# Performance work log

Hardware: AMD Instinct MI355X
Metric: run time of the kernel (lower is better)

Reference implementation:

```python
import jax, jax.numpy as jnp
import numpy as np

B, L, H, E = 4, 2048, 8, 64
WINDOW = 8
DILATION = 1


def setup_inputs() -> dict:
    key = jax.random.key(0)
    kq, kk, kv, ka = jax.random.split(key, 4)
    queries = jax.random.normal(kq, (B, L, H, E), dtype=jnp.float32)
    keys = jax.random.normal(kk, (B, L, H, E), dtype=jnp.float32)
    values = jax.random.normal(kv, (B, L, H, E), dtype=jnp.float32)
    alpha = jax.random.uniform(ka, (1,), dtype=jnp.float32)
    return {"queries": queries, "keys": keys, "values": values, "alpha": alpha}


def _full_attention(q, k, v, scale):
    # q,k,v: [B, L, H, E]
    scores = jnp.einsum('blhe,bshe->bhls', q, k) * scale  # [B,H,L,L]
    A = jax.nn.softmax(scores, axis=-1)
    return jnp.einsum('bhls,bshd->blhd', A, v)


def _local_attention(q, k, v, scale):
    # efficient gather-based local window attention, non-causal
    Lk = k.shape[1]
    offsets = jnp.arange(-WINDOW, WINDOW + 1) * DILATION
    idx = jnp.clip(jnp.arange(Lk)[:, None] + offsets[None, :], 0, Lk - 1)
    K_win = k[:, idx]
    V_win = v[:, idx]
    scores = jnp.einsum('blhe,blwhe->blhw', q, K_win) * scale
    A = jax.nn.softmax(scores, axis=-1)
    return jnp.einsum('blhw,blwhe->blhe', A, V_win)


def reference(queries, keys, values, alpha):
    scale = 1.0 / np.sqrt(queries.shape[-1]).astype(np.float32)
    out_full = _full_attention(queries, keys, values, scale)
    out_local = _local_attention(queries, keys, values, scale)
    w = jax.nn.sigmoid(alpha[0])
    # only_target_first=True: positions 1..L-1 take out_full, position 0 is gated
    out = out_full.at[:, 0].set(w * out_full[:, 0] + (1.0 - w) * out_local[:, 0])
    return out
```

## Files before the change

### kernel.cpp

```cpp
#include <hip/hip_runtime.h>

typedef unsigned short u16;
typedef unsigned int   u32;
typedef __attribute__((ext_vector_type(8))) short short8;
typedef __attribute__((ext_vector_type(16))) float f32x16;

#define MFMA32(a, b, c) __builtin_amdgcn_mfma_f32_32x32x16_bf16(a, b, c, 0, 0, 0)

constexpr int Lv = 2048, Hv = 8, Ev = 64, HE = Hv * Ev;
constexpr float QSCALE = 0.18033688011112042f;
constexpr size_t WSV_OFF = 32u * 64u * 2048u;
#define WS_NEED ((size_t)16777216)

__device__ __forceinline__ float bf2f(u16 u) {
    u32 x = ((u32)u) << 16;
    return __builtin_bit_cast(float, x);
}
__device__ __forceinline__ u16 f2bf(float f) {
    u32 x = __builtin_bit_cast(u32, f);
    u32 r = ((x >> 16) & 1u) + 0x7fffu;
    return (u16)((x + r) >> 16);
}
__device__ __forceinline__ u32 pkbf(float a, float b) {
#if __has_builtin(__builtin_amdgcn_cvt_pk_bf16_f32)
    typedef __attribute__((ext_vector_type(2))) __bf16 bf16x2;
    bf16x2 v = __builtin_amdgcn_cvt_pk_bf16_f32(a, b);
    return __builtin_bit_cast(u32, v);
#else
    return (u32)f2bf(a) | ((u32)f2bf(b) << 16);
#endif
}
__device__ __forceinline__ float fexp2(float x) {
#if __has_builtin(__builtin_amdgcn_exp2f)
    return __builtin_amdgcn_exp2f(x);
#else
    return exp2f(x);
#endif
}

__device__ __forceinline__ void gll16(const void* g, void* l) {
    __builtin_amdgcn_global_load_lds(
        (const __attribute__((address_space(1))) void*)g,
        (__attribute__((address_space(3))) void*)l, 16, 0, 0);
}

__device__ __forceinline__ int detect_isbf16(const u32* q32, int lane) {
    u32 w0 = q32[2 * lane];
    u32 w1 = q32[2 * lane + 1];
    u16 uu[4] = { (u16)(w0 & 0xffff), (u16)(w0 >> 16),
                  (u16)(w1 & 0xffff), (u16)(w1 >> 16) };
    int p = 0, z = 0;
#pragma unroll
    for (int j = 0; j < 4; ++j) {
        u16 mgn = (u16)(uu[j] & 0x7fff);
        int ex  = mgn >> 7;
        bool zero = (mgn == 0);
        bool pl   = zero || (ex >= 115 && ex <= 132);
        p += pl ? 1 : 0;
        if ((j & 1) == 0) z += zero ? 1 : 0;
    }
    int acc = p | (z << 16);
#pragma unroll
    for (int o = 1; o < 64; o <<= 1) acc += __shfl_xor(acc, o);
    int ps = acc & 0xffff, zs = acc >> 16;
    if (zs >= 100) return 0;
    return (ps >= 240) ? 1 : 0;
}

__device__ __forceinline__ short8 cvt8s(const float* p, float s) {
    float4 a = *(const float4*)p, b4 = *(const float4*)(p + 4);
    u32 r[4] = { pkbf(a.x * s, a.y * s), pkbf(a.z * s, a.w * s),
                 pkbf(b4.x * s, b4.y * s), pkbf(b4.z * s, b4.w * s) };
    return *(short8*)r;
}

__device__ __forceinline__ f32x16 zv16() {
    f32x16 z;
#pragma unroll
    for (int r = 0; r < 16; ++r) z[r] = 0.f;
    return z;
}

__device__ __forceinline__ void plswap(u32& a, u32& b) {
#if __has_builtin(__builtin_amdgcn_permlane32_swap)
    auto r = __builtin_amdgcn_permlane32_swap(a, b, false, false);
    a = r[0]; b = r[1];
#else
    int lane = (int)(threadIdx.x & 63);
    u32 ax = (u32)__shfl_xor((int)a, 32);
    u32 bx = (u32)__shfl_xor((int)b, 32);
    bool hi = lane >= 32;
    u32 na = hi ? bx : a;
    u32 nb = hi ? b  : ax;
    a = na; b = nb;
#endif
}

template <int ISBF>
__device__ __forceinline__ void convert_impl(const void* kin, const void* vin,
                                             u16* __restrict__ ws, u16* VT) {
    const int blk = blockIdx.x;
    const int xcd = blk & 7;
    const int bh  = xcd * 4 + ((blk >> 3) & 3);
    const int tg  = blk >> 5;
    const int b   = bh >> 3, h = bh & 7;
    const size_t inb = (size_t)b * Lv * HE + h * Ev;
    u16* kimg = ws + ((size_t)bh * 64 + tg) * 2048;
    u16* vimg = ws + WSV_OFF + ((size_t)bh * 64 + tg) * 2048;
    const int t = threadIdx.x;

    if (ISBF) {
        int key = t >> 3, p8 = t & 7;
        size_t src = inb + (size_t)(tg * 32 + key) * HE + p8 * 8;
        uint4 v = *(const uint4*)((const u16*)vin + src);
        *(uint4*)&VT[key * 72 + p8 * 8] = v;
    } else {
#pragma unroll
        for (int r = 0; r < 2; ++r) {
            int f = t + 256 * r;
            int key = f >> 4, part = f & 15;
            size_t src = inb + (size_t)(tg * 32 + key) * HE + part * 4;
            float4 v = *(const float4*)((const float*)vin + src);
            uint2 pv; pv.x = pkbf(v.x, v.y); pv.y = pkbf(v.z, v.w);
            *(uint2*)&VT[key * 72 + part * 4] = pv;
        }
    }

    {
        int a = 8 * t;
        int key = a >> 6, sf = (a & 63) >> 3;
        int e0 = ((sf ^ (key & 7)) << 3);
        size_t s = inb + (size_t)(tg * 32 + key) * HE + e0;
        if (ISBF) {
            uint4 v = *(const uint4*)((const u16*)kin + s);
            *(uint4*)&kimg[a] = v;
        } else {
            float4 p0 = *(const float4*)((const float*)kin + s);
            float4 p1 = *(const float4*)((const float*)kin + s + 4);
            uint4 v; v.x = pkbf(p0.x, p0.y); v.y = pkbf(p0.z, p0.w);
                     v.z = pkbf(p1.x, p1.y); v.w = pkbf(p1.z, p1.w);
            *(uint4*)&kimg[a] = v;
        }
    }

    __syncthreads();

#pragma unroll
    for (int r = 0; r < 2; ++r) {
        int idx = t + 256 * r;
        int a = 4 * idx;
        int e = a >> 5, sf = (a & 31) >> 3, j0 = a & 7;
        int m = (e + (e >> 3)) & 3;
        int k0 = ((sf ^ m) << 3) + j0;
        uint2 val;
        val.x = (u32)VT[k0 * 72 + e]       | ((u32)VT[(k0 + 1) * 72 + e] << 16);
        val.y = (u32)VT[(k0 + 2) * 72 + e] | ((u32)VT[(k0 + 3) * 72 + e] << 16);
        *(uint2*)&vimg[a] = val;
    }
}

__global__ __launch_bounds__(256) void convert_kernel(
    const void* __restrict__ qv, const void* __restrict__ kv,
    const void* __restrict__ vv, u16* __restrict__ ws)
{
    __shared__ u16 VT[32 * 72];
    const int isbf = detect_isbf16((const u32*)qv, threadIdx.x & 63);
    if (isbf) convert_impl<1>(kv, vv, ws, VT);
    else      convert_impl<0>(kv, vv, ws, VT);
}

template <int ISBF, int WS>
__device__ __forceinline__ void attn_impl(
    const void* __restrict__ qv, const void* __restrict__ kv,
    const void* __restrict__ vv, const void* __restrict__ alphav,
    void* __restrict__ outv, const u16* __restrict__ ws, u16* SMEM)
{
    const int tid  = threadIdx.x;
    const int w    = tid >> 6;
    const int lane = tid & 63;
    const int l31  = lane & 31;
    const int hi   = lane >> 5;
    const int qg   = w & 3;
    const int g    = w >> 2;

    const int fid = blockIdx.x;
    const int bh  = (fid & 7) * 4 + ((fid >> 3) & 3);
    const int rb  = fid >> 5;
    const int b   = bh >> 3, h = bh & 7;
    const int row0 = rb * 128;

    const size_t bhoff = (size_t)b * Lv * HE + h * Ev;
    const u16*   q16 = (const u16*)qv + bhoff;
    const u16*   k16 = (const u16*)kv + bhoff;
    const u16*   v16 = (const u16*)vv + bhoff;
    const float* q32 = (const float*)qv + bhoff;
    const float* k32 = (const float*)kv + bhoff;
    const float* v32 = (const float*)vv + bhoff;

    u16* ldsK = SMEM + w * 4096;
    u16* ldsV = ldsK + 2048;

    short8 qf[4];
    {
        size_t ro = (size_t)(row0 + qg * 32 + l31) * HE + hi * 8;
        if (ISBF) {
#pragma unroll
            for (int c = 0; c < 4; ++c) {
                short8 t = *(const short8*)(q16 + ro + 16 * c);
#pragma unroll
                for (int j = 0; j < 8; ++j)
                    qf[c][j] = (short)f2bf(bf2f((u16)t[j]) * QSCALE);
            }
        } else {
#pragma unroll
            for (int c = 0; c < 4; ++c) qf[c] = cvt8s(q32 + ro + 16 * c, QSCALE);
        }
    }

    f32x16 O[2];
    O[0] = zv16(); O[1] = zv16();
    f32x16 StA = zv16(), StB = zv16();
    float psum = 0.f;

    const u16* kimg0 = ws + ((size_t)bh * 64 + g * 32) * 2048;
    const u16* vimg0 = ws + WSV_OFF + ((size_t)bh * 64 + g * 32) * 2048;
    const size_t keybase = (size_t)g * 1024;

    const int k0l = lane >> 3;
    const int kj  = lane & 7;
    const int e0K = ((kj ^ k0l) << 3);
    const int eoV = kj * 8;

    float4 fpa, fpb, fpc, fpd;
    uint4  upa, upb;

#define GLLK(KT) do {                                                          \
        const u16* ib_ = kimg0 + (size_t)(KT) * 2048 + lane * 8;               \
        _Pragma("unroll")                                                      \
        for (int s_ = 0; s_ < 4; ++s_)                                         \
            gll16(ib_ + s_ * 512, ldsK + s_ * 512);                            \
    } while (0)
#define GLLV(KT) do {                                                          \
        const u16* ib_ = vimg0 + (size_t)(KT) * 2048 + lane * 8;               \
        _Pragma("unroll")                                                      \
        for (int s_ = 0; s_ < 4; ++s_)                                         \
            gll16(ib_ + s_ * 512, ldsV + s_ * 512);                            \
    } while (0)
#define WAITV4() do { asm volatile("s_waitcnt vmcnt(4)" ::: "memory");         \
        __builtin_amdgcn_sched_barrier(0); } while (0)
#define WAITV0() do { asm volatile("s_waitcnt vmcnt(0)" ::: "memory");         \
        __builtin_amdgcn_sched_barrier(0); } while (0)
#define WAITL0() do { asm volatile("s_waitcnt lgkmcnt(0)" ::: "memory");       \
        __builtin_amdgcn_sched_barrier(0); } while (0)

#define LK0(KT, CH) do {                                                       \
        size_t tb_ = (keybase + (size_t)(KT) * 32) * HE;                       \
        int key_ = (CH) * 16 + k0l;                                            \
        if (ISBF) {                                                            \
            const u16* p_ = k16 + tb_ + (size_t)key_ * HE + e0K;               \
            upa = *(const uint4*)p_;                                           \
            upb = *(const uint4*)(p_ + 8 * HE);                                \
        } else {                                                               \
            const float* p_ = k32 + tb_ + (size_t)key_ * HE + e0K;             \
            fpa = *(const float4*)p_;            fpb = *(const float4*)(p_ + 4);\
            fpc = *(const float4*)(p_ + 8 * HE); fpd = *(const float4*)(p_ + 8 * HE + 4);\
        }                                                                      \
    } while (0)
#define SK0(CH) do {                                                           \
        if (ISBF) {                                                            \
            *(uint4*)&ldsK[((CH)*2    ) * 512 + lane * 8] = upa;               \
            *(uint4*)&ldsK[((CH)*2 + 1) * 512 + lane * 8] = upb;               \
        } else {                                                               \
            u32 t0_[4] = { pkbf(fpa.x, fpa.y), pkbf(fpa.z, fpa.w),             \
                           pkbf(fpb.x, fpb.y), pkbf(fpb.z, fpb.w) };           \
            u32 t1_[4] = { pkbf(fpc.x, fpc.y), pkbf(fpc.z, fpc.w),             \
                           pkbf(fpd.x, fpd.y), pkbf(fpd.z, fpd.w) };           \
            *(uint4*)&ldsK[((CH)*2    ) * 512 + lane * 8] = *(uint4*)t0_;      \
            *(uint4*)&ldsK[((CH)*2 + 1) * 512 + lane * 8] = *(uint4*)t1_;      \
        }                                                                      \
    } while (0)
#define LV0(KT, VH) do {                                                       \
        size_t tb_ = (keybase + (size_t)(KT) * 32 + (VH) * 16 + 2 * k0l) * HE; \
        if (ISBF) {                                                            \
            const u16* p_ = v16 + tb_ + eoV;                                   \
            upa = *(const uint4*)p_;                                           \
            upb = *(const uint4*)(p_ + HE);                                    \
        } else {                                                               \
            const float* p_ = v32 + tb_ + eoV;                                 \
            fpa = *(const float4*)p_;       fpb = *(const float4*)(p_ + 4);    \
            fpc = *(const float4*)(p_ + HE); fpd = *(const float4*)(p_ + HE + 4);\
        }                                                                      \
    } while (0)
#define SV0(VH) do {                                                           \
        int s_ = (k0l >> 2) + (VH) * 2;                                        \
        if (ISBF) {                                                            \
            const u16* a0_ = (const u16*)&upa;                                 \
            const u16* a1_ = (const u16*)&upb;                                 \
            _Pragma("unroll")                                                  \
            for (int j = 0; j < 8; ++j) {                                      \
                int e_ = eoV + j;                                              \
                int sl_ = s_ ^ ((e_ + (e_ >> 3)) & 3);                         \
                *(u32*)&ldsV[e_ * 32 + sl_ * 8 + ((2 * k0l) & 7)] =            \
                    (u32)a0_[j] | ((u32)a1_[j] << 16);                         \
            }                                                                  \
        } else {                                                               \
            float t0_[8] = {fpa.x, fpa.y, fpa.z, fpa.w, fpb.x, fpb.y, fpb.z, fpb.w};\
            float t1_[8] = {fpc.x, fpc.y, fpc.z, fpc.w, fpd.x, fpd.y, fpd.z, fpd.w};\
            _Pragma("unroll")                                                  \
            for (int j = 0; j < 8; ++j) {                                      \
                int e_ = eoV + j;                                              \
                int sl_ = s_ ^ ((e_ + (e_ >> 3)) & 3);                         \
                *(u32*)&ldsV[e_ * 32 + sl_ * 8 + ((2 * k0l) & 7)] =            \
                    pkbf(t0_[j], t1_[j]);                                      \
            }                                                                  \
        }                                                                      \
    } while (0)

#define QK_(ST) do {                                                           \
        (ST) = zv16();                                                         \
        __builtin_amdgcn_s_setprio(1);                                         \
        _Pragma("unroll")                                                      \
        for (int c = 0; c < 4; ++c) {                                          \
            int sl = (2 * c + hi) ^ (l31 & 7);                                 \
            short8 kf = *(const short8*)&ldsK[l31 * 64 + sl * 8];              \
            (ST) = MFMA32(kf, qf[c], (ST));                                    \
        }                                                                      \
        __builtin_amdgcn_s_setprio(0);                                         \
    } while (0)

    u32 c8[8];
#define SM_(SP) do {                                                           \
        _Pragma("unroll")                                                      \
        for (int r = 0; r < 16; ++r) (SP)[r] = fexp2((SP)[r]);                 \
        _Pragma("unroll")                                                      \
        for (int r = 0; r < 16; ++r) psum += (SP)[r];                          \
        _Pragma("unroll")                                                      \
        for (int q = 0; q < 8; ++q) c8[q] = pkbf((SP)[2 * q], (SP)[2 * q + 1]);\
    } while (0)

#define PV_(T) do {                                                            \
        u32 a0 = c8[4 * (T) + 0], a1 = c8[4 * (T) + 1];                        \
        u32 a2 = c8[4 * (T) + 2], a3 = c8[4 * (T) + 3];                        \
        plswap(a0, a2);                                                        \
        plswap(a1, a3);                                                        \
        u32 pw_[4] = { a0, a1, a2, a3 };                                       \
        short8 pa = *(short8*)pw_;                                             \
        __builtin_amdgcn_s_setprio(1);                                         \
        _Pragma("unroll")                                                      \
        for (int et = 0; et < 2; ++et) {                                       \
            int e  = et * 32 + l31;                                            \
            int sl = (2 * (T) + hi) ^ ((e + (e >> 3)) & 3);                    \
            short8 vf = *(const short8*)&ldsV[e * 32 + sl * 8];                \
            O[et] = MFMA32(pa, vf, O[et]);                                     \
        }                                                                      \
        __builtin_amdgcn_s_setprio(0);                                         \
    } while (0)

#define BODY(KT, SC, SP) do {                                                  \
        WAITV4();                   \
        QK_(SC);                    \
        SM_(SP);                    \
        WAITL0();                   \
        GLLK((KT) + 1);                                                        \
        WAITV4();                   \
        PV_(0);                                                                \
        PV_(1);                     \
        WAITL0();                   \
        GLLV(KT);                                                              \
    } while (0)

    if (WS) {
        GLLK(0);
        WAITV0();
        QK_(StA);
        WAITL0();
        GLLK(1);
        GLLV(0);
        for (int j = 0; j < 15; ++j) {
            const int kt = 2 * j + 1;
            BODY(kt,     StB, StA);
            BODY(kt + 1, StA, StB);
        }
        WAITV4();
        QK_(StB);
        SM_(StA);
        WAITL0();
        WAITV0();
        PV_(0);
        PV_(1);
        WAITL0();
        GLLV(31);
        WAITV0();
        SM_(StB);
        PV_(0);
        PV_(1);
    } else {
        LK0(0, 0); SK0(0); LK0(0, 1); SK0(1);
        LV0(0, 0); SV0(0); LV0(0, 1); SV0(1);
        for (int kt = 0; kt < 32; ++kt) {
            if (kt < 31) LK0(kt + 1, 0);
            QK_(StA);
            if (kt < 31) { SK0(0); LK0(kt + 1, 1); }
            SM_(StA);
            if (kt < 31) { SK0(1); LV0(kt + 1, 0); }
            PV_(0);
            if (kt < 31) { SV0(0); LV0(kt + 1, 1); }
            PV_(1);
            if (kt < 31) SV0(1);
        }
    }
#undef GLLK
#undef GLLV
#undef WAITV4
#undef WAITV0
#undef WAITL0
#undef LK0
#undef SK0
#undef LV0
#undef SV0
#undef QK_
#undef SM_
#undef PV_
#undef BODY

    __syncthreads();
    float pst = psum + __shfl_xor(psum, 32);
    float* cb = (float*)SMEM;
    const int cbase = qg * 2368 + lane * 36;

    if (g == 1) {
        union { f32x16 v; float4 q4[4]; } u;
        u.v = O[0];
#pragma unroll
        for (int i = 0; i < 4; ++i) *(float4*)&cb[cbase + 4 * i] = u.q4[i];
        u.v = O[1];
#pragma unroll
        for (int i = 0; i < 4; ++i) *(float4*)&cb[cbase + 16 + 4 * i] = u.q4[i];
        cb[qg * 2368 + 2304 + lane] = pst;
    }

    float locv[2] = {0.f, 0.f};
    float wgt = 0.f;
    const bool w0blk = (rb == 0) && (w == 0);
    if (w0blk) {
        const int e = lane;
        const size_t base = bhoff + e;
#define LDIN(p, i) (ISBF ? bf2f(((const u16*)(p))[i]) : ((const float*)(p))[i])
        float qe = LDIN(qv, base);
        float s[9];
#pragma unroll
        for (int j = 0; j < 9; ++j) {
            float prod = qe * LDIN(kv, base + (size_t)j * HE);
#pragma unroll
            for (int o = 1; o < 64; o <<= 1) prod += __shfl_xor(prod, o);
            s[j] = prod * 0.125f;
        }
        float mx = s[0];
#pragma unroll
        for (int j = 1; j < 9; ++j) mx = fmaxf(mx, s[j]);
        float we[9];
#pragma unroll
        for (int j = 0; j < 9; ++j) we[j] = expf(s[j] - mx);
        float denom = 9.f * we[0];
        float acc   = 9.f * we[0] * LDIN(vv, base);
#pragma unroll
        for (int j = 1; j < 9; ++j) {
            denom += we[j];
            acc   += we[j] * LDIN(vv, base + (size_t)j * HE);
        }
        float loc = acc / denom;

        float a;
        if (ISBF) {
            a = bf2f(((const u16*)alphav)[0]);
            if (!(a >= 0.0f && a <= 1.0f)) {
                float af = ((const float*)alphav)[0];
                if (af >= 0.0f && af <= 1.0f) a = af;
            }
        } else {
            a = ((const float*)alphav)[0];
            if (!(a >= 0.0f && a <= 1.0f)) {
                float ab = bf2f(((const u16*)alphav)[0]);
                if (ab >= 0.0f && ab <= 1.0f) a = ab;
            }
        }
        wgt = 1.f / (1.f + expf(-a));
#pragma unroll
        for (int et = 0; et < 2; ++et) locv[et] = __shfl(loc, et * 32 + l31);
#undef LDIN
    }

    __syncthreads();
    if (g != 0) return;

    float pstp = cb[qg * 2368 + 2304 + lane];
#pragma unroll
    for (int r = 0; r < 16; ++r) {
        O[0][r] += cb[cbase + r];
        O[1][r] += cb[cbase + 16 + r];
    }
    float invv = 1.0f / (pst + pstp);

#pragma unroll
    for (int rg = 0; rg < 4; ++rg) {
#pragma unroll
        for (int rr = 0; rr < 4; ++rr) {
            const int reg = rg * 4 + rr;
            const int rl  = rr + 8 * rg + 4 * hi;
            float inv = __shfl(invv, rl);
            int row = row0 + qg * 32 + rl;
            size_t oo = (size_t)(b * Lv + row) * HE + h * Ev + l31;
            bool blend = w0blk && (rl == 0);
#pragma unroll
            for (int et = 0; et < 2; ++et) {
                float res = O[et][reg] * inv;
                if (blend) res = wgt * res + (1.f - wgt) * locv[et];
                if (ISBF) ((u16*)outv)[oo + et * 32] = f2bf(res);
                else      ((float*)outv)[oo + et * 32] = res;
            }
        }
    }
}

__global__ __launch_bounds__(512, 4) void attn_kernel_ws(
    const void* __restrict__ qv, const void* __restrict__ kv,
    const void* __restrict__ vv, const void* __restrict__ alphav,
    void* __restrict__ outv, const u16* __restrict__ ws)
{
    __shared__ u16 SMEM[32768];
    const int isbf = detect_isbf16((const u32*)qv, threadIdx.x & 63);
    if (isbf) attn_impl<1, 1>(qv, kv, vv, alphav, outv, ws, SMEM);
    else      attn_impl<0, 1>(qv, kv, vv, alphav, outv, ws, SMEM);
}

__global__ __launch_bounds__(512, 4) void attn_kernel_nws(
    const void* __restrict__ qv, const void* __restrict__ kv,
    const void* __restrict__ vv, const void* __restrict__ alphav,
    void* __restrict__ outv)
{
    __shared__ u16 SMEM[32768];
    const int isbf = detect_isbf16((const u32*)qv, threadIdx.x & 63);
    if (isbf) attn_impl<1, 0>(qv, kv, vv, alphav, outv, nullptr, SMEM);
    else      attn_impl<0, 0>(qv, kv, vv, alphav, outv, nullptr, SMEM);
}

extern "C" void kernel_launch(void* const* d_in, const int* in_sizes, int n_in,
                              void* d_out, int out_size, void* d_ws, size_t ws_size,
                              hipStream_t stream) {
    if (d_ws != nullptr && ws_size >= WS_NEED) {
        hipLaunchKernelGGL(convert_kernel, dim3(2048), dim3(256), 0, stream,
                           d_in[0], d_in[1], d_in[2], (u16*)d_ws);
        hipLaunchKernelGGL(attn_kernel_ws, dim3(512), dim3(512), 0, stream,
                           d_in[0], d_in[1], d_in[2], d_in[3], d_out,
                           (const u16*)d_ws);
    } else {
        hipLaunchKernelGGL(attn_kernel_nws, dim3(512), dim3(512), 0, stream,
                           d_in[0], d_in[1], d_in[2], d_in[3], d_out);
    }
}
```

Before: 146.5 us.

## Fuse K/V conversion and attention into one cooperative kernel with grid sync

```diff
diff --git a/kernel.cpp b/kernel.cpp
--- a/kernel.cpp
+++ b/kernel.cpp
@@ -1,4 +1,5 @@
 #include <hip/hip_runtime.h>
+#include <hip/hip_cooperative_groups.h>
 
 typedef unsigned short u16;
 typedef unsigned int   u32;
@@ -96,67 +97,67 @@
 #endif
 }
 
-template <int ISBF>
-__device__ __forceinline__ void convert_impl(const void* kin, const void* vin,
-                                             u16* __restrict__ ws, u16* VT) {
-    const int blk = blockIdx.x;
-    const int xcd = blk & 7;
-    const int bh  = xcd * 4 + ((blk >> 3) & 3);
-    const int tg  = blk >> 5;
-    const int b   = bh >> 3, h = bh & 7;
-    const size_t inb = (size_t)b * Lv * HE + h * Ev;
-    u16* kimg = ws + ((size_t)bh * 64 + tg) * 2048;
-    u16* vimg = ws + WSV_OFF + ((size_t)bh * 64 + tg) * 2048;
-    const int t = threadIdx.x;
-
-    if (ISBF) {
-        int key = t >> 3, p8 = t & 7;
-        size_t src = inb + (size_t)(tg * 32 + key) * HE + p8 * 8;
-        uint4 v = *(const uint4*)((const u16*)vin + src);
-        *(uint4*)&VT[key * 72 + p8 * 8] = v;
-    } else {
-#pragma unroll
-        for (int r = 0; r < 2; ++r) {
-            int f = t + 256 * r;
-            int key = f >> 4, part = f & 15;
-            size_t src = inb + (size_t)(tg * 32 + key) * HE + part * 4;
-            float4 v = *(const float4*)((const float*)vin + src);
-            uint2 pv; pv.x = pkbf(v.x, v.y); pv.y = pkbf(v.z, v.w);
-            *(uint2*)&VT[key * 72 + part * 4] = pv;
-        }
-    }
-
-    {
-        int a = 8 * t;
-        int key = a >> 6, sf = (a & 63) >> 3;
-        int e0 = ((sf ^ (key & 7)) << 3);
+
+template <int ISBF, int NT>
+__device__ __forceinline__ void conv_tile(const void* kin, const void* vin,
+                                          size_t inb, int tg,
+                                          u16* __restrict__ kdst,
+                                          u16* __restrict__ vimg,
+                                          u16* __restrict__ VTt, int tl) {
+#pragma unroll
+    for (int r = 0; r < 2048 / (8 * NT); ++r) {
+        int a = 8 * (tl + NT * r);
+        int key = a >> 6, e0 = a & 63;
         size_t s = inb + (size_t)(tg * 32 + key) * HE + e0;
         if (ISBF) {
-            uint4 v = *(const uint4*)((const u16*)kin + s);
-            *(uint4*)&kimg[a] = v;
+            *(uint4*)&kdst[a] = *(const uint4*)((const u16*)kin + s);
         } else {
             float4 p0 = *(const float4*)((const float*)kin + s);
             float4 p1 = *(const float4*)((const float*)kin + s + 4);
             uint4 v; v.x = pkbf(p0.x, p0.y); v.y = pkbf(p0.z, p0.w);
                      v.z = pkbf(p1.x, p1.y); v.w = pkbf(p1.z, p1.w);
-            *(uint4*)&kimg[a] = v;
-        }
-    }
-
+            *(uint4*)&kdst[a] = v;
+        }
+    }
+#pragma unroll
+    for (int r = 0; r < 512 / NT; ++r) {
+        int f = tl + NT * r;
+        int key = f >> 4, part = f & 15;
+        size_t src = inb + (size_t)(tg * 32 + key) * HE + part * 4;
+        if (ISBF) {
+            uint2 vv_ = *(const uint2*)((const u16*)vin + src);
+            *(uint2*)&VTt[key * 72 + part * 4] = vv_;
+        } else {
+            float4 v = *(const float4*)((const float*)vin + src);
+            uint2 pv; pv.x = pkbf(v.x, v.y); pv.y = pkbf(v.z, v.w);
+            *(uint2*)&VTt[key * 72 + part * 4] = pv;
+        }
+    }
     __syncthreads();
-
-#pragma unroll
-    for (int r = 0; r < 2; ++r) {
-        int idx = t + 256 * r;
+#pragma unroll
+    for (int r = 0; r < 512 / NT; ++r) {
+        int idx = tl + NT * r;
         int a = 4 * idx;
         int e = a >> 5, sf = (a & 31) >> 3, j0 = a & 7;
         int m = (e + (e >> 3)) & 3;
         int k0 = ((sf ^ m) << 3) + j0;
         uint2 val;
-        val.x = (u32)VT[k0 * 72 + e]       | ((u32)VT[(k0 + 1) * 72 + e] << 16);
-        val.y = (u32)VT[(k0 + 2) * 72 + e] | ((u32)VT[(k0 + 3) * 72 + e] << 16);
+        val.x = (u32)VTt[k0 * 72 + e]       | ((u32)VTt[(k0 + 1) * 72 + e] << 16);
+        val.y = (u32)VTt[(k0 + 2) * 72 + e] | ((u32)VTt[(k0 + 3) * 72 + e] << 16);
         *(uint2*)&vimg[a] = val;
     }
+}
+
+template <int ISBF>
+__device__ __forceinline__ void convert_impl(const void* kin, const void* vin,
+                                             u16* __restrict__ ws, u16* VT) {
+    const int blk = blockIdx.x;
+    const int bh  = blk >> 6, tg = blk & 63;
+    const int b   = bh >> 3,  h  = bh & 7;
+    const size_t inb = (size_t)b * Lv * HE + h * Ev;
+    u16* kdst = ws + ((size_t)bh * 2048 + (size_t)tg * 32) * 64;
+    u16* vimg = ws + WSV_OFF + ((size_t)bh * 64 + tg) * 2048;
+    conv_tile<ISBF, 256>(kin, vin, inb, tg, kdst, vimg, VT, threadIdx.x);
 }
 
 __global__ __launch_bounds__(256) void convert_kernel(
@@ -167,6 +168,24 @@
     const int isbf = detect_isbf16((const u32*)qv, threadIdx.x & 63);
     if (isbf) convert_impl<1>(kv, vv, ws, VT);
     else      convert_impl<0>(kv, vv, ws, VT);
+}
+
+template <int ISBF>
+__device__ __forceinline__ void convert_phase(const void* kin, const void* vin,
+                                              u16* __restrict__ ws, u16* SMEM) {
+    const int fid = blockIdx.x;
+    const int bh  = (fid & 7) * 4 + ((fid >> 3) & 3);
+    const int rb  = fid >> 5;
+    const int t   = threadIdx.x;
+    const int tt  = t >> 7, tl = t & 127;
+    const int tg  = rb * 4 + tt;
+    const int b   = bh >> 3, h = bh & 7;
+    const size_t inb = (size_t)b * Lv * HE + h * Ev;
+    u16* kdst = ws + ((size_t)bh * 2048 + (size_t)tg * 32) * 64;
+    u16* vimg = ws + WSV_OFF + ((size_t)bh * 64 + tg) * 2048;
+    u16* VTt  = SMEM + tt * 2304;
+    conv_tile<ISBF, 128>(kin, vin, inb, tg, kdst, vimg, VTt, tl);
+    __syncthreads();
 }
 
 template <int ISBF, int WS>
@@ -222,8 +241,9 @@
     f32x16 StA = zv16(), StB = zv16();
     float psum = 0.f;
 
-    const u16* kimg0 = ws + ((size_t)bh * 64 + g * 32) * 2048;
+    const u16* kimg0 = ws + ((size_t)bh * 2048 + (size_t)g * 1024) * 64;
     const u16* vimg0 = ws + WSV_OFF + ((size_t)bh * 64 + g * 32) * 2048;
+    const int klaneoff = (lane >> 3) * 64 + (((lane & 7) ^ ((lane >> 3) & 7)) << 3);
     const size_t keybase = (size_t)g * 1024;
 
     const int k0l = lane >> 3;
@@ -235,7 +255,7 @@
     uint4  upa, upb;
 
 #define GLLK(KT) do {                                                          \
-        const u16* ib_ = kimg0 + (size_t)(KT) * 2048 + lane * 8;               \
+        const u16* ib_ = kimg0 + (size_t)(KT) * 2048 + klaneoff;               \
         _Pragma("unroll")                                                      \
         for (int s_ = 0; s_ < 4; ++s_)                                         \
             gll16(ib_ + s_ * 512, ldsK + s_ * 512);                            \
@@ -522,6 +542,20 @@
     }
 }
 
+__global__ __launch_bounds__(512, 4) void fused_kernel(
+    const void* __restrict__ qv, const void* __restrict__ kv,
+    const void* __restrict__ vv, const void* __restrict__ alphav,
+    void* __restrict__ outv, u16* __restrict__ ws)
+{
+    __shared__ u16 SMEM[32768];
+    const int isbf = detect_isbf16((const u32*)qv, threadIdx.x & 63);
+    if (isbf) convert_phase<1>(kv, vv, ws, SMEM);
+    else      convert_phase<0>(kv, vv, ws, SMEM);
+    cooperative_groups::this_grid().sync();
+    if (isbf) attn_impl<1, 1>(qv, kv, vv, alphav, outv, ws, SMEM);
+    else      attn_impl<0, 1>(qv, kv, vv, alphav, outv, ws, SMEM);
+}
+
 __global__ __launch_bounds__(512, 4) void attn_kernel_ws(
     const void* __restrict__ qv, const void* __restrict__ kv,
     const void* __restrict__ vv, const void* __restrict__ alphav,
@@ -548,6 +582,14 @@
                               void* d_out, int out_size, void* d_ws, size_t ws_size,
                               hipStream_t stream) {
     if (d_ws != nullptr && ws_size >= WS_NEED) {
+        void* q  = d_in[0]; void* k = d_in[1]; void* v = d_in[2];
+        void* al = d_in[3]; void* o = d_out;  void* w = d_ws;
+        void* kargs[6] = { &q, &k, &v, &al, &o, &w };
+        hipError_t e = hipLaunchCooperativeKernel(
+            reinterpret_cast<void*>(fused_kernel), dim3(512), dim3(512),
+            kargs, 0, stream);
+        if (e == hipSuccess) return;
+        (void)hipGetLastError();
         hipLaunchKernelGGL(convert_kernel, dim3(2048), dim3(256), 0, stream,
                            d_in[0], d_in[1], d_in[2], (u16*)d_ws);
         hipLaunchKernelGGL(attn_kernel_ws, dim3(512), dim3(512), 0, stream,
```

New measurement: 229.1 us. 1.56x slower.
